# Kernel tuning notes

Measured on AMD Instinct MI355X. Metric: run time of the kernel, lower is better.

Reference implementation:

```python
import jax, jax.numpy as jnp
import numpy as np

B, T = 64, 512
V, E, H, L = 256, 512, 1024, 4
D = max(H // 2, V)  # decoder hidden = 512


def setup_inputs() -> dict:
    key = jax.random.key(0)
    ks = jax.random.split(key, 12)
    s = 1.0 / np.sqrt(H)  # torch GRUCell uniform(-1/sqrt(H), 1/sqrt(H)) init
    return {
        "token_indices": jax.random.randint(ks[0], (B, T), 0, V, dtype=jnp.int32),
        "embed": jax.random.normal(ks[1], (V, E), dtype=jnp.float32),
        "W_ih": jax.random.uniform(ks[2], (L, 3 * H, H + E), jnp.float32, -s, s),
        "W_hh": jax.random.uniform(ks[3], (L, 3 * H, H), jnp.float32, -s, s),
        "b_ih": jax.random.uniform(ks[4], (L, 3 * H), jnp.float32, -s, s),
        "b_hh": jax.random.uniform(ks[5], (L, 3 * H), jnp.float32, -s, s),
        "h0": jax.random.uniform(ks[6], (L, H), jnp.float32),  # torch.rand
        "dec_W1": jax.random.normal(ks[7], (H, D), jnp.float32) * 0.02,
        "dec_b1": jnp.zeros((D,), jnp.float32),
        "dec_W2": jax.random.normal(ks[8], (D, V), jnp.float32) * 0.02,
        "dec_b2": jnp.zeros((V,), jnp.float32),
    }


def reference(token_indices, embed, W_ih, W_hh, b_ih, b_hh, h0, dec_W1, dec_b1, dec_W2, dec_b2):
    Bn = token_indices.shape[0]
    e = embed[token_indices].transpose(1, 0, 2)  # [T, B, E]
    h_init = jnp.broadcast_to(h0[:, None, :], (L, Bn, H))  # each layer's own hidden

    def step(h, e_t):
        # every layer gets concat([own hidden, token embed]) -- layers are independent
        x = jnp.concatenate([h, jnp.broadcast_to(e_t[None], (L, Bn, E))], axis=-1)  # [L,B,H+E]
        gi = jnp.einsum('lbi,lgi->lbg', x, W_ih) + b_ih[:, None, :]  # [L,B,3H]
        gh = jnp.einsum('lbh,lgh->lbg', h, W_hh) + b_hh[:, None, :]
        ir, iz, inn = jnp.split(gi, 3, axis=-1)
        hr, hz, hn = jnp.split(gh, 3, axis=-1)
        r = jax.nn.sigmoid(ir + hr)
        z = jax.nn.sigmoid(iz + hz)
        n = jnp.tanh(inn + r * hn)
        h_new = (1.0 - z) * n + z * h
        return h_new, h_new[-1]  # only top layer feeds the decoder

    _, tops = jax.lax.scan(step, h_init, e)  # [T, B, H]
    hdec = jax.nn.relu(jnp.einsum('tbh,hd->tbd', tops, dec_W1) + dec_b1)
    logits = jnp.einsum('tbd,dv->tbv', hdec, dec_W2) + dec_b2  # [T, B, V]
    return logits.transpose(1, 0, 2)  # [B, T, V]
```

## Files before the change

### kernel.cpp

```cpp
#include <hip/hip_runtime.h>
#include <cstdint>
#include <cstddef>

typedef _Float16 half8 __attribute__((ext_vector_type(8)));
typedef float f32x4 __attribute__((ext_vector_type(4)));

#define WIH3_OFF 14155776
#define WHH3_OFF 9437184

__global__ __launch_bounds__(256) void prep_misc_kernel(
    const float* __restrict__ embed, const float* __restrict__ W_ih,
    const float* __restrict__ dec_W1, const float* __restrict__ dec_W2,
    const float* __restrict__ b_ih, const float* __restrict__ b_hh,
    const float* __restrict__ h0,
    _Float16* __restrict__ embed16, _Float16* __restrict__ wihe16,
    _Float16* __restrict__ w1t16, _Float16* __restrict__ w2t16,
    float* __restrict__ te_bias, float* __restrict__ h32, _Float16* __restrict__ h16,
    unsigned int* __restrict__ bar)
{
  int i = blockIdx.x * 256 + threadIdx.x;
  if (i < 131072) { embed16[i] = (_Float16)embed[i]; return; }
  i -= 131072;
  if (i < 1572864) {
    int r = i >> 9, e = i & 511;
    wihe16[i] = (_Float16)W_ih[WIH3_OFF + r * 1536 + 1024 + e]; return;
  }
  i -= 1572864;
  if (i < 524288) {
    int d = i >> 10, h = i & 1023;
    w1t16[i] = (_Float16)dec_W1[h * 512 + d]; return;
  }
  i -= 524288;
  if (i < 131072) {
    int v = i >> 9, d = i & 511;
    w2t16[i] = (_Float16)dec_W2[d * 256 + v]; return;
  }
  i -= 131072;
  if (i < 3072) {
    te_bias[i] = b_ih[9216 + i] + (i < 2048 ? b_hh[9216 + i] : 0.f); return;
  }
  i -= 3072;
  if (i < 65536) {
    float v = h0[3072 + (i & 1023)];
    h32[i] = v; h16[i] = (_Float16)v; return;
  }
  i -= 65536;
  if (i < 65536) { bar[i] = 0u; return; }
}

__global__ __launch_bounds__(256) void prep_u_kernel(
    const float* __restrict__ W_ih, const float* __restrict__ W_hh,
    _Float16* __restrict__ U16)
{
  int i = blockIdx.x * 256 + threadIdx.x;
  int row = i >> 10, k = i & 1023;
  int j = row >> 2, g = row & 3;
  const float* Wih3 = W_ih + WIH3_OFF;
  const float* Whh3 = W_hh + WHH3_OFF;
  float v;
  if (g == 0)      v = Wih3[j * 1536 + k] + Whh3[j * 1024 + k];
  else if (g == 1) v = Wih3[(1024 + j) * 1536 + k] + Whh3[(1024 + j) * 1024 + k];
  else if (g == 2) v = Wih3[(2048 + j) * 1536 + k];
  else             v = Whh3[(2048 + j) * 1024 + k];
  U16[i] = (_Float16)v;
}

__device__ __forceinline__ void gld_lds16(const void* g, void* l) {
  __builtin_amdgcn_global_load_lds(
      (const __attribute__((address_space(1))) unsigned int*)g,
      (__attribute__((address_space(3))) unsigned int*)l, 16, 0, 0);
}

__global__ __launch_bounds__(256) void gemm_bt_kernel(
    const _Float16* __restrict__ A, const _Float16* __restrict__ Bt,
    const float* __restrict__ bias, float* __restrict__ outF,
    _Float16* __restrict__ outH, int M, int N, int K, int mode, int t0)
{
  __shared__ _Float16 As[128 * 32];
  __shared__ _Float16 Bs[128 * 32];
  int tid = threadIdx.x, lane = tid & 63, wave = tid >> 6;
  int nbn = N >> 7;
  int bm = blockIdx.x / nbn, bn = blockIdx.x % nbn;
  int m0 = bm << 7, n0 = bn << 7;
  int wm = wave & 1, wn = wave >> 1;

  f32x4 acc[4][4];
#pragma unroll
  for (int i = 0; i < 4; i++)
#pragma unroll
    for (int j = 0; j < 4; j++) { f32x4 z = {0.f, 0.f, 0.f, 0.f}; acc[i][j] = z; }

  int aoff = ((wm << 6) + (lane & 15)) * 32 + ((lane >> 4) << 3);
  int boff = ((wn << 6) + (lane & 15)) * 32 + ((lane >> 4) << 3);

  for (int kt = 0; kt < K; kt += 32) {
    __syncthreads();
#pragma unroll
    for (int p = 0; p < 2; ++p) {
      int s = (p << 8) + tid;
      int row = s >> 2, seg = s & 3;
      char* ldsA = (char*)As + (p << 12) + (wave << 10);
      char* ldsB = (char*)Bs + (p << 12) + (wave << 10);
      gld_lds16(A + (size_t)(m0 + row) * K + kt + seg * 8, ldsA);
      gld_lds16(Bt + (size_t)(n0 + row) * K + kt + seg * 8, ldsB);
    }
    __syncthreads();
    half8 af[4], bf[4];
#pragma unroll
    for (int i = 0; i < 4; ++i) af[i] = *(const half8*)&As[aoff + i * 512];
#pragma unroll
    for (int j = 0; j < 4; ++j) bf[j] = *(const half8*)&Bs[boff + j * 512];
#pragma unroll
    for (int i = 0; i < 4; ++i)
#pragma unroll
      for (int j = 0; j < 4; ++j)
        acc[i][j] = __builtin_amdgcn_mfma_f32_16x16x32_f16(af[i], bf[j], acc[i][j], 0, 0, 0);
  }

#pragma unroll
  for (int i = 0; i < 4; ++i) {
    int mbase = m0 + (wm << 6) + (i << 4) + ((lane >> 4) << 2);
#pragma unroll
    for (int j = 0; j < 4; ++j) {
      int n = n0 + (wn << 6) + (j << 4) + (lane & 15);
      float bv = bias[n];
#pragma unroll
      for (int r = 0; r < 4; ++r) {
        float v = acc[i][j][r] + bv;
        int mm = mbase + r;
        if (mode == 0)      outF[(size_t)mm * N + n] = v;
        else if (mode == 1) outH[(size_t)mm * N + n] = (_Float16)fmaxf(v, 0.f);
        else {
          int tt = t0 + (mm >> 6), b = mm & 63;
          outF[((size_t)b * 512 + tt) * 256 + n] = v;
        }
      }
    }
  }
}

__global__ __launch_bounds__(256, 1) void recur_kernel(
    const _Float16* __restrict__ U16, const float* __restrict__ Te,
    const int* __restrict__ tokens, const float* __restrict__ b_hh,
    float* __restrict__ h32, _Float16* __restrict__ h16,
    _Float16* __restrict__ tops, unsigned int* __restrict__ bar, int t0, int t1)
{
  __shared__ _Float16 hs[16 * 1032];
  __shared__ float gates[16 * 68];
  __shared__ unsigned char ltok[16 * 512];
  __shared__ _Float16 hrep[16 * 24];

  int tid = threadIdx.x, lane = tid & 63, w = tid >> 6;
  int rg = blockIdx.x >> 2, bg = blockIdx.x & 3;

  for (int i = tid; i < 8192; i += 256)
    ltok[i] = (unsigned char)tokens[((bg << 4) + (i >> 9)) * 512 + (i & 511)];

  half8 Bf[32];
  {
    const _Float16* Ub = U16 + (size_t)((rg << 6) + (w << 4) + (lane & 15)) * 1024 + ((lane >> 4) << 3);
#pragma unroll
    for (int kt = 0; kt < 32; ++kt) Bf[kt] = *(const half8*)(Ub + (kt << 5));
  }

  int lb = tid >> 4, jl = tid & 15;
  int j = (rg << 4) + jl;
  int b = (bg << 4) + lb;
  float bhhn = b_hh[11264 + j];
  float hold = h32[(b << 10) + j];
  const float* tebase = Te + j;
  __syncthreads();

  const _Float16* hsA = &hs[(lane & 15) * 1032 + ((lane >> 4) << 3)];
  int srow = tid >> 6, scol = tid & 63;

  for (int t = t0; t < t1; ++t) {
    {
      const _Float16* gsrc = h16 + (size_t)(t & 1) * 65536 + ((size_t)bg << 14)
                             + ((size_t)srow << 10) + (scol << 3);
      f32x4 r0, r1, r2, r3, r4, r5, r6, r7;
      asm volatile(
        "global_load_dwordx4 %0, %8, off sc0 sc1\n\t"
        "global_load_dwordx4 %1, %9, off sc0 sc1\n\t"
        "global_load_dwordx4 %2, %10, off sc0 sc1\n\t"
        "global_load_dwordx4 %3, %11, off sc0 sc1\n\t"
        "global_load_dwordx4 %4, %12, off sc0 sc1\n\t"
        "global_load_dwordx4 %5, %13, off sc0 sc1\n\t"
        "global_load_dwordx4 %6, %14, off sc0 sc1\n\t"
        "global_load_dwordx4 %7, %15, off sc0 sc1\n\t"
        "s_waitcnt vmcnt(0)"
        : "=&v"(r0), "=&v"(r1), "=&v"(r2), "=&v"(r3),
          "=&v"(r4), "=&v"(r5), "=&v"(r6), "=&v"(r7)
        : "v"(gsrc), "v"(gsrc + 512), "v"(gsrc + 4096), "v"(gsrc + 4608),
          "v"(gsrc + 8192), "v"(gsrc + 8704), "v"(gsrc + 12288), "v"(gsrc + 12800)
        : "memory");
      _Float16* ldst = &hs[srow * 1032 + (scol << 3)];
      *(f32x4*)(ldst)          = r0;  *(f32x4*)(ldst + 512)   = r1;
      *(f32x4*)(ldst + 4128)   = r2;  *(f32x4*)(ldst + 4640)  = r3;
      *(f32x4*)(ldst + 8256)   = r4;  *(f32x4*)(ldst + 8768)  = r5;
      *(f32x4*)(ldst + 12384)  = r6;  *(f32x4*)(ldst + 12896) = r7;
    }
    __syncthreads();

    f32x4 a0 = {0.f, 0.f, 0.f, 0.f}, a1 = {0.f, 0.f, 0.f, 0.f};
#pragma unroll
    for (int kt = 0; kt < 32; kt += 2) {
      half8 x0 = *(const half8*)(hsA + (kt << 5));
      half8 x1 = *(const half8*)(hsA + (kt << 5) + 32);
      a0 = __builtin_amdgcn_mfma_f32_16x16x32_f16(x0, Bf[kt], a0, 0, 0, 0);
      a1 = __builtin_amdgcn_mfma_f32_16x16x32_f16(x1, Bf[kt + 1], a1, 0, 0, 0);
    }
    f32x4 acc = a0 + a1;
    int lr = (w << 4) + (lane & 15);
#pragma unroll
    for (int r = 0; r < 4; ++r)
      gates[(((lane >> 4) << 2) + r) * 68 + lr] = acc[r];
    __syncthreads();

    float4 g = *(const float4*)&gates[lb * 68 + (jl << 2)];
    int tok = ltok[(lb << 9) + t];
    const float* te = tebase + tok * 3072;
    float te0 = te[0], te1 = te[1024], te2 = te[2048];
    float rr = 1.f / (1.f + __expf(-(g.x + te0)));
    float zz = 1.f / (1.f + __expf(-(g.y + te1)));
    float nv = tanhf(g.z + te2 + rr * (g.w + bhhn));
    float hnew = (1.f - zz) * nv + zz * hold;
    hold = hnew;
    hrep[lb * 24 + jl] = (_Float16)hnew;
    __syncthreads();

    if (tid < 32) {
      int wb = tid >> 1, c = tid & 1;
      f32x4 v = *(const f32x4*)&hrep[wb * 24 + (c << 3)];
      _Float16* dst = h16 + (size_t)((t + 1) & 1) * 65536
                      + ((size_t)(((bg << 4) + wb)) << 10) + (rg << 4) + (c << 3);
      asm volatile("global_store_dwordx4 %0, %1, off sc0 sc1" :: "v"(dst), "v"(v) : "memory");
      *(f32x4*)(tops + ((size_t)(t - t0) << 16)
                + ((size_t)(((bg << 4) + wb)) << 10) + (rg << 4) + (c << 3)) = v;
    }
    asm volatile("s_waitcnt vmcnt(0)" ::: "memory");
    __syncthreads();

    if (tid < 8) {
      unsigned int* line = bar + (t << 7) + (tid << 4);
      if (tid == (int)(blockIdx.x & 7))
        __hip_atomic_fetch_add(line, 1u, __ATOMIC_RELAXED, __HIP_MEMORY_SCOPE_AGENT);
      while (__hip_atomic_load(line, __ATOMIC_RELAXED, __HIP_MEMORY_SCOPE_AGENT) != 32u) {}
    }
    __syncthreads();
  }
  h32[(b << 10) + j] = hold;
}

extern "C" void kernel_launch(void* const* d_in, const int* in_sizes, int n_in,
                              void* d_out, int out_size, void* d_ws, size_t ws_size,
                              hipStream_t stream) {
  const int*   tokens = (const int*)d_in[0];
  const float* embed  = (const float*)d_in[1];
  const float* W_ih   = (const float*)d_in[2];
  const float* W_hh   = (const float*)d_in[3];
  const float* b_ih   = (const float*)d_in[4];
  const float* b_hh   = (const float*)d_in[5];
  const float* h0     = (const float*)d_in[6];
  const float* dec_W1 = (const float*)d_in[7];
  const float* dec_b1 = (const float*)d_in[8];
  const float* dec_W2 = (const float*)d_in[9];
  const float* dec_b2 = (const float*)d_in[10];
  float* out = (float*)d_out;
  (void)in_sizes; (void)n_in; (void)out_size;

  char* ws = (char*)d_ws;
  size_t off = 0;
  auto alloc = [&](size_t bytes) -> char* {
    char* p = ws + off;
    off = (off + bytes + 255) & ~(size_t)255;
    return p;
  };
  _Float16* U16     = (_Float16*)alloc((size_t)4096 * 1024 * 2);
  float*    Te      = (float*)alloc((size_t)256 * 3072 * 4);
  float*    te_bias = (float*)alloc(3072 * 4);
  _Float16* embed16 = (_Float16*)alloc(131072 * 2);
  _Float16* wihe16  = (_Float16*)alloc((size_t)1572864 * 2);
  _Float16* w1t16   = (_Float16*)alloc(524288 * 2);
  _Float16* w2t16   = (_Float16*)alloc(131072 * 2);
  float*    h32     = (float*)alloc(65536 * 4);
  _Float16* h16     = (_Float16*)alloc((size_t)2 * 65536 * 2);
  unsigned int* bar = (unsigned int*)alloc((size_t)65536 * 4);
  size_t fixed = off;

  size_t per_t = (size_t)(65536 + 32768) * 2;
  long remain = (long)ws_size - (long)fixed - 1024;
  int chunk_T = remain > 0 ? (int)(remain / (long)per_t) : 0;
  chunk_T &= ~1;
  if (chunk_T > 512) chunk_T = 512;
  if (chunk_T < 2) chunk_T = 2;
  _Float16* tops = (_Float16*)alloc((size_t)chunk_T * 65536 * 2);
  _Float16* hdec = (_Float16*)alloc((size_t)chunk_T * 32768 * 2);

  prep_misc_kernel<<<9740, 256, 0, stream>>>(embed, W_ih, dec_W1, dec_W2, b_ih, b_hh, h0,
                                             embed16, wihe16, w1t16, w2t16, te_bias, h32, h16, bar);
  prep_u_kernel<<<16384, 256, 0, stream>>>(W_ih, W_hh, U16);
  gemm_bt_kernel<<<2 * 24, 256, 0, stream>>>(embed16, wihe16, te_bias, Te, nullptr,
                                             256, 3072, 512, 0, 0);

  for (int t0 = 0; t0 < 512; t0 += chunk_T) {
    int t1 = t0 + chunk_T; if (t1 > 512) t1 = 512;
    void* args[] = {&U16, &Te, (void*)&tokens, (void*)&b_hh, &h32, &h16, &tops, &bar, &t0, &t1};
    hipLaunchCooperativeKernel((const void*)recur_kernel, dim3(256), dim3(256), args, 0, stream);
    int Mc = (t1 - t0) * 64;
    gemm_bt_kernel<<<(Mc / 128) * 4, 256, 0, stream>>>(tops, w1t16, dec_b1, nullptr, hdec,
                                                       Mc, 512, 1024, 1, 0);
    gemm_bt_kernel<<<(Mc / 128) * 2, 256, 0, stream>>>(hdec, w2t16, dec_b2, out, nullptr,
                                                       Mc, 256, 512, 2, t0);
  }
}
```

Before: 2.709 ms.

## Split recurrent matvec over K across waves with swizzled LDS and partial-sum reduction

```diff
diff --git a/kernel.cpp b/kernel.cpp
--- a/kernel.cpp
+++ b/kernel.cpp
@@ -145,9 +145,9 @@
     float* __restrict__ h32, _Float16* __restrict__ h16,
     _Float16* __restrict__ tops, unsigned int* __restrict__ bar, int t0, int t1)
 {
-  __shared__ _Float16 hs[16 * 1032];
-  __shared__ float gates[16 * 68];
-  __shared__ unsigned char ltok[16 * 512];
+  __shared__ _Float16 hs[16384];
+  __shared__ float part[4 * 64 * 20];
+  __shared__ unsigned char ltok[8192];
   __shared__ _Float16 hrep[16 * 24];
 
   int tid = threadIdx.x, lane = tid & 63, w = tid >> 6;
@@ -156,11 +156,15 @@
   for (int i = tid; i < 8192; i += 256)
     ltok[i] = (unsigned char)tokens[((bg << 4) + (i >> 9)) * 512 + (i & 511)];
 
-  half8 Bf[32];
+  half8 Bf[4][8];
   {
-    const _Float16* Ub = U16 + (size_t)((rg << 6) + (w << 4) + (lane & 15)) * 1024 + ((lane >> 4) << 3);
-#pragma unroll
-    for (int kt = 0; kt < 32; ++kt) Bf[kt] = *(const half8*)(Ub + (kt << 5));
+    const _Float16* Ub = U16 + (size_t)((rg << 6) + (lane & 15)) * 1024
+                         + (w << 8) + ((lane >> 4) << 3);
+#pragma unroll
+    for (int rt = 0; rt < 4; ++rt)
+#pragma unroll
+      for (int kt = 0; kt < 8; ++kt)
+        Bf[rt][kt] = *(const half8*)(Ub + rt * 16384 + (kt << 5));
   }
 
   int lb = tid >> 4, jl = tid & 15;
@@ -169,15 +173,17 @@
   float bhhn = b_hh[11264 + j];
   float hold = h32[(b << 10) + j];
   const float* tebase = Te + j;
+
+  int srow0 = tid >> 7;
+  int ccol  = tid & 127;
+  int cx    = ccol & 15;
+  int c0    = (w << 5) + (lane >> 4);
   __syncthreads();
-
-  const _Float16* hsA = &hs[(lane & 15) * 1032 + ((lane >> 4) << 3)];
-  int srow = tid >> 6, scol = tid & 63;
 
   for (int t = t0; t < t1; ++t) {
     {
-      const _Float16* gsrc = h16 + (size_t)(t & 1) * 65536 + ((size_t)bg << 14)
-                             + ((size_t)srow << 10) + (scol << 3);
+      const _Float16* gb = h16 + (size_t)(t & 1) * 65536 + ((size_t)bg << 14)
+                           + (srow0 << 10) + (ccol << 3);
       f32x4 r0, r1, r2, r3, r4, r5, r6, r7;
       asm volatile(
         "global_load_dwordx4 %0, %8, off sc0 sc1\n\t"
@@ -191,55 +197,78 @@
         "s_waitcnt vmcnt(0)"
         : "=&v"(r0), "=&v"(r1), "=&v"(r2), "=&v"(r3),
           "=&v"(r4), "=&v"(r5), "=&v"(r6), "=&v"(r7)
-        : "v"(gsrc), "v"(gsrc + 512), "v"(gsrc + 4096), "v"(gsrc + 4608),
-          "v"(gsrc + 8192), "v"(gsrc + 8704), "v"(gsrc + 12288), "v"(gsrc + 12800)
+        : "v"(gb), "v"(gb + 2048), "v"(gb + 4096), "v"(gb + 6144),
+          "v"(gb + 8192), "v"(gb + 10240), "v"(gb + 12288), "v"(gb + 14336)
         : "memory");
-      _Float16* ldst = &hs[srow * 1032 + (scol << 3)];
-      *(f32x4*)(ldst)          = r0;  *(f32x4*)(ldst + 512)   = r1;
-      *(f32x4*)(ldst + 4128)   = r2;  *(f32x4*)(ldst + 4640)  = r3;
-      *(f32x4*)(ldst + 8256)   = r4;  *(f32x4*)(ldst + 8768)  = r5;
-      *(f32x4*)(ldst + 12384)  = r6;  *(f32x4*)(ldst + 12896) = r7;
-    }
-    __syncthreads();
-
-    f32x4 a0 = {0.f, 0.f, 0.f, 0.f}, a1 = {0.f, 0.f, 0.f, 0.f};
-#pragma unroll
-    for (int kt = 0; kt < 32; kt += 2) {
-      half8 x0 = *(const half8*)(hsA + (kt << 5));
-      half8 x1 = *(const half8*)(hsA + (kt << 5) + 32);
-      a0 = __builtin_amdgcn_mfma_f32_16x16x32_f16(x0, Bf[kt], a0, 0, 0, 0);
-      a1 = __builtin_amdgcn_mfma_f32_16x16x32_f16(x1, Bf[kt + 1], a1, 0, 0, 0);
-    }
-    f32x4 acc = a0 + a1;
-    int lr = (w << 4) + (lane & 15);
-#pragma unroll
-    for (int r = 0; r < 4; ++r)
-      gates[(((lane >> 4) << 2) + r) * 68 + lr] = acc[r];
-    __syncthreads();
-
-    float4 g = *(const float4*)&gates[lb * 68 + (jl << 2)];
+      _Float16* lb0 = &hs[ccol << 7];
+      *(f32x4*)(lb0 + (((srow0     ) ^ cx) << 3)) = r0;
+      *(f32x4*)(lb0 + (((srow0 +  2) ^ cx) << 3)) = r1;
+      *(f32x4*)(lb0 + (((srow0 +  4) ^ cx) << 3)) = r2;
+      *(f32x4*)(lb0 + (((srow0 +  6) ^ cx) << 3)) = r3;
+      *(f32x4*)(lb0 + (((srow0 +  8) ^ cx) << 3)) = r4;
+      *(f32x4*)(lb0 + (((srow0 + 10) ^ cx) << 3)) = r5;
+      *(f32x4*)(lb0 + (((srow0 + 12) ^ cx) << 3)) = r6;
+      *(f32x4*)(lb0 + (((srow0 + 14) ^ cx) << 3)) = r7;
+    }
+    __syncthreads();
+
+    half8 af[8];
+#pragma unroll
+    for (int kt = 0; kt < 8; ++kt) {
+      int c = c0 + (kt << 2);
+      af[kt] = *(const half8*)&hs[(c << 7) + (((lane & 15) ^ (c & 15)) << 3)];
+    }
+    f32x4 a0 = {0.f,0.f,0.f,0.f}, a1 = a0, a2 = a0, a3 = a0;
+#pragma unroll
+    for (int kt = 0; kt < 8; ++kt) {
+      a0 = __builtin_amdgcn_mfma_f32_16x16x32_f16(af[kt], Bf[0][kt], a0, 0, 0, 0);
+      a1 = __builtin_amdgcn_mfma_f32_16x16x32_f16(af[kt], Bf[1][kt], a1, 0, 0, 0);
+      a2 = __builtin_amdgcn_mfma_f32_16x16x32_f16(af[kt], Bf[2][kt], a2, 0, 0, 0);
+      a3 = __builtin_amdgcn_mfma_f32_16x16x32_f16(af[kt], Bf[3][kt], a3, 0, 0, 0);
+    }
+    {
+      int l = lane & 15, q = lane >> 4;
+      *(f32x4*)&part[(w * 1280) + (l      ) * 20 + (q << 2)] = a0;
+      *(f32x4*)&part[(w * 1280) + (l + 16) * 20 + (q << 2)] = a1;
+      *(f32x4*)&part[(w * 1280) + (l + 32) * 20 + (q << 2)] = a2;
+      *(f32x4*)&part[(w * 1280) + (l + 48) * 20 + (q << 2)] = a3;
+    }
+    __syncthreads();
+
+    float g0 = 0.f, g1 = 0.f, g2 = 0.f, g3 = 0.f;
+    int rowb = jl << 2;
+#pragma unroll
+    for (int ww = 0; ww < 4; ++ww) {
+      const float* pb = &part[ww * 1280 + rowb * 20 + lb];
+      g0 += pb[0]; g1 += pb[20]; g2 += pb[40]; g3 += pb[60];
+    }
     int tok = ltok[(lb << 9) + t];
     const float* te = tebase + tok * 3072;
     float te0 = te[0], te1 = te[1024], te2 = te[2048];
-    float rr = 1.f / (1.f + __expf(-(g.x + te0)));
-    float zz = 1.f / (1.f + __expf(-(g.y + te1)));
-    float nv = tanhf(g.z + te2 + rr * (g.w + bhhn));
+    float rr = 1.f / (1.f + __expf(-(g0 + te0)));
+    float zz = 1.f / (1.f + __expf(-(g1 + te1)));
+    float xx = g2 + te2 + rr * (g3 + bhhn);
+    float e2 = __expf(2.f * xx);
+    float nv = 1.f - 2.f / (e2 + 1.f);
     float hnew = (1.f - zz) * nv + zz * hold;
     hold = hnew;
     hrep[lb * 24 + jl] = (_Float16)hnew;
     __syncthreads();
 
     if (tid < 32) {
-      int wb = tid >> 1, c = tid & 1;
-      f32x4 v = *(const f32x4*)&hrep[wb * 24 + (c << 3)];
+      int wb = tid >> 1, cc = tid & 1;
+      f32x4 v = *(const f32x4*)&hrep[wb * 24 + (cc << 3)];
       _Float16* dst = h16 + (size_t)((t + 1) & 1) * 65536
-                      + ((size_t)(((bg << 4) + wb)) << 10) + (rg << 4) + (c << 3);
+                      + ((size_t)((bg << 4) + wb) << 10) + (rg << 4) + (cc << 3);
       asm volatile("global_store_dwordx4 %0, %1, off sc0 sc1" :: "v"(dst), "v"(v) : "memory");
+    }
+    asm volatile("s_waitcnt vmcnt(0)" ::: "memory");
+    if (tid >= 64 && tid < 96) {
+      int wb = (tid - 64) >> 1, cc = tid & 1;
+      f32x4 v = *(const f32x4*)&hrep[wb * 24 + (cc << 3)];
       *(f32x4*)(tops + ((size_t)(t - t0) << 16)
-                + ((size_t)(((bg << 4) + wb)) << 10) + (rg << 4) + (c << 3)) = v;
-    }
-    asm volatile("s_waitcnt vmcnt(0)" ::: "memory");
-    __syncthreads();
+                + ((size_t)((bg << 4) + wb) << 10) + (rg << 4) + (cc << 3)) = v;
+    }
 
     if (tid < 8) {
       unsigned int* line = bar + (t << 7) + (tid << 4);
```

New measurement: 2.292 ms. 1.18x faster.
